# Kernel optimization log

Measured on AMD Instinct MI355X. Metric: run time of the kernel, lower is better.

The kernel has to match this reference:

```python
import jax, jax.numpy as jnp
import numpy as np
import math

D_MODEL = 1024
NUM_HEADS = 16
D_K = D_MODEL // NUM_HEADS
MAX_LEN = 2048
BATCH = 2
SEQ = 2048


def setup_inputs() -> dict:
    key = jax.random.key(0)
    ks = jax.random.split(key, 12)
    w_scale = 0.02  # realistic init scale for linear weights
    inp = {
        "q": jax.random.normal(ks[0], (BATCH, SEQ, D_MODEL), jnp.float32),
        "k": jax.random.normal(ks[1], (BATCH, SEQ, D_MODEL), jnp.float32),
        "v": jax.random.normal(ks[2], (BATCH, SEQ, D_MODEL), jnp.float32),
        # learned params
        "rel_emb": jax.random.normal(ks[3], (2 * MAX_LEN, D_K), jnp.float32),
        "wq": jax.random.normal(ks[4], (D_MODEL, D_MODEL), jnp.float32) * w_scale,
        "bq": jnp.zeros((D_MODEL,), jnp.float32),
        "wk": jax.random.normal(ks[5], (D_MODEL, D_MODEL), jnp.float32) * w_scale,
        "bk": jnp.zeros((D_MODEL,), jnp.float32),
        "wv": jax.random.normal(ks[6], (D_MODEL, D_MODEL), jnp.float32) * w_scale,
        "bv": jnp.zeros((D_MODEL,), jnp.float32),
        "wo": jax.random.normal(ks[7], (D_MODEL, D_MODEL), jnp.float32) * w_scale,
        "bo": jnp.zeros((D_MODEL,), jnp.float32),
    }
    return inp


def reference(q, k, v, rel_emb, wq, bq, wk, bk, wv, bv, wo, bo):
    B, L, D = q.shape
    H, dk = NUM_HEADS, D // NUM_HEADS

    def split_heads(x):  # [B, L, D] -> [B, H, L, dk]
        return x.reshape(B, L, H, dk).transpose(0, 2, 1, 3)

    qh = split_heads(q @ wq.T + bq)
    kh = split_heads(k @ wk.T + bk)
    vh = split_heads(v @ wv.T + bv)

    # relative positions: rel_pos[i, j] = (j - i) + MAX_LEN, in [0, 2*MAX_LEN)
    r = jnp.arange(L)
    rel_pos = r[None, :] - r[:, None] + MAX_LEN  # [L, L] int32

    content_score = jnp.einsum("bhid,bhjd->bhij", qh, kh)
    # pos_score[b,h,i,j] = q[b,h,i,:] . rel_emb[rel_pos[i,j], :]
    rel = rel_emb[rel_pos]  # [L, L, dk]
    pos_score = jnp.einsum("bhid,ijd->bhij", qh, rel)

    scores = (content_score + pos_score) / math.sqrt(dk)
    attn = jax.nn.softmax(scores, axis=-1)
    out = jnp.einsum("bhij,bhjd->bhid", attn, vh)  # [B, H, L, dk]
    out = out.transpose(0, 2, 1, 3).reshape(B, L, D)
    return out @ wo.T + bo
```

## Files before the change

### kernel.cpp

```cpp
#include <hip/hip_runtime.h>
#include <hip/hip_fp16.h>


typedef _Float16 f16;
typedef _Float16 f16x4 __attribute__((ext_vector_type(4)));
typedef _Float16 f16x8 __attribute__((ext_vector_type(8)));
typedef float    f32x4 __attribute__((ext_vector_type(4)));

#define NBATCH 2
#define NHEADS 16
#define DKDIM  64
#define SEQL   2048
#define DMODEL 1024
#define NTOK   4096
#define MAXLEN 2048

__global__ void cvt_f32_f16(const float* __restrict__ src, f16* __restrict__ dst, int n4) {
    int i = blockIdx.x * blockDim.x + threadIdx.x;
    if (i < n4) {
        float4 v = ((const float4*)src)[i];
        f16x4 h = { (f16)v.x, (f16)v.y, (f16)v.z, (f16)v.w };
        ((f16x4*)dst)[i] = h;
    }
}

__global__ __launch_bounds__(256) void qkv_proj(
    const float* __restrict__ qg, const float* __restrict__ kg, const float* __restrict__ vg,
    const float* __restrict__ wq, const float* __restrict__ wk, const float* __restrict__ wv,
    const float* __restrict__ bq, const float* __restrict__ bk, const float* __restrict__ bv,
    f16* __restrict__ qh, f16* __restrict__ kh, f16* __restrict__ vt)
{
    const int which = blockIdx.z;
    const float* X    = which == 0 ? qg : (which == 1 ? kg : vg);
    const float* W    = which == 0 ? wq : (which == 1 ? wk : wv);
    const float* bias = which == 0 ? bq : (which == 1 ? bk : bv);

    __shared__ f16 As[128][72];
    __shared__ f16 Bs[128][72];

    const int tid = threadIdx.x;
    const int lane = tid & 63;
    const int w = tid >> 6;
    const int wr = w >> 1, wc = w & 1;
    const int row0 = blockIdx.y * 128;
    const int col0 = blockIdx.x * 128;

    f32x4 acc[4][4] = {};

    for (int kk = 0; kk < DMODEL; kk += 64) {
        #pragma unroll
        for (int rep = 0; rep < 8; ++rep) {
            int idx = rep * 256 + tid;
            int r = idx >> 4, seg = idx & 15;
            float4 va = *(const float4*)&X[(size_t)(row0 + r) * DMODEL + kk + seg * 4];
            f16x4 ha = { (f16)va.x, (f16)va.y, (f16)va.z, (f16)va.w };
            *(f16x4*)&As[r][seg * 4] = ha;
            float4 vb = *(const float4*)&W[(size_t)(col0 + r) * DMODEL + kk + seg * 4];
            f16x4 hb = { (f16)vb.x, (f16)vb.y, (f16)vb.z, (f16)vb.w };
            *(f16x4*)&Bs[r][seg * 4] = hb;
        }
        __syncthreads();

        f16x8 a[4][2], b[4][2];
        #pragma unroll
        for (int mi = 0; mi < 4; ++mi)
            #pragma unroll
            for (int ks = 0; ks < 2; ++ks)
                a[mi][ks] = *(const f16x8*)&As[wr * 64 + mi * 16 + (lane & 15)][ks * 32 + (lane >> 4) * 8];
        #pragma unroll
        for (int ni = 0; ni < 4; ++ni)
            #pragma unroll
            for (int ks = 0; ks < 2; ++ks)
                b[ni][ks] = *(const f16x8*)&Bs[wc * 64 + ni * 16 + (lane & 15)][ks * 32 + (lane >> 4) * 8];
        __builtin_amdgcn_s_setprio(1);
        #pragma unroll
        for (int mi = 0; mi < 4; ++mi)
            #pragma unroll
            for (int ni = 0; ni < 4; ++ni)
                #pragma unroll
                for (int ks = 0; ks < 2; ++ks)
                    acc[mi][ni] = __builtin_amdgcn_mfma_f32_16x16x32_f16(a[mi][ks], b[ni][ks], acc[mi][ni], 0, 0, 0);
        __builtin_amdgcn_s_setprio(0);
        __syncthreads();
    }

    #pragma unroll
    for (int mi = 0; mi < 4; ++mi) {
        #pragma unroll
        for (int ni = 0; ni < 4; ++ni) {
            int col = col0 + wc * 64 + ni * 16 + (lane & 15);
            int h = col >> 6, d = col & 63;
            float bc = bias[col];
            #pragma unroll
            for (int r = 0; r < 4; ++r) {
                int row = row0 + wr * 64 + mi * 16 + (lane >> 4) * 4 + r;
                int b_ = row >> 11, l = row & 2047;
                float val = acc[mi][ni][r] + bc;
                if (which == 0)
                    qh[((size_t)((b_ * 16 + h) * 2048 + l)) * 64 + d] = (f16)val;
                else if (which == 1)
                    kh[((size_t)((b_ * 16 + h) * 2048 + l)) * 64 + d] = (f16)val;
                else
                    vt[((size_t)((b_ * 16 + h) * 64 + d)) * 2048 + l] = (f16)val;
            }
        }
    }
}

__global__ __launch_bounds__(256, 3) void flash_attn(
    const f16* __restrict__ qh, const f16* __restrict__ kh, const f16* __restrict__ vt,
    const f16* __restrict__ rel, f16* __restrict__ att)
{
    const int tid = threadIdx.x, lane = tid & 63, w = tid >> 6;
    const int bh = blockIdx.y;
    const int b = bh >> 4, h = bh & 15;
    const int i0 = blockIdx.x * 64;

    __shared__ f16 Ks[64][72];
    __shared__ f16 Vs[64][72];
    __shared__ f16 Rb[128][72];
    __shared__ f16 Qb[4][16][88];

    const size_t base_kq = (size_t)bh * SEQL * DKDIM;
    const int pb0 = MAXLEN - i0 - 63;

    #pragma unroll
    for (int rep = 0; rep < 2; ++rep) {
        int idx = rep * 256 + tid;
        int r = idx >> 3, seg = idx & 7;
        *(int4*)&Ks[r][seg * 8] = *(const int4*)&qh[base_kq + (size_t)(i0 + r) * 64 + seg * 8];
        int p = pb0 + r;
        *(int4*)&Rb[p & 127][seg * 8] = *(const int4*)&rel[(size_t)p * 64 + seg * 8];
    }
    __syncthreads();
    f16x8 aq[2];
    aq[0] = *(const f16x8*)&Ks[w * 16 + (lane & 15)][(lane >> 4) * 8];
    aq[1] = *(const f16x8*)&Ks[w * 16 + (lane & 15)][32 + (lane >> 4) * 8];
    __syncthreads();

    float mrun[4], lrun[4];
    f32x4 oacc[4] = {};
    #pragma unroll
    for (int r = 0; r < 4; ++r) { mrun[r] = -1e30f; lrun[r] = 0.f; }

    const int p0w_off = 48 - w * 16;

    for (int j0 = 0; j0 < SEQL; j0 += 64) {
        #pragma unroll
        for (int rep = 0; rep < 2; ++rep) {
            int idx = rep * 256 + tid;
            int r = idx >> 3, seg = idx & 7;
            *(int4*)&Ks[r][seg * 8] = *(const int4*)&kh[base_kq + (size_t)(j0 + r) * 64 + seg * 8];
            *(int4*)&Vs[r][seg * 8] = *(const int4*)&vt[base_kq + (size_t)r * 2048 + j0 + seg * 8];
            int p = pb0 + j0 + 64 + r;
            int slot = p & 127;
            if (p > 4095) p = 4095;
            *(int4*)&Rb[slot][seg * 8] = *(const int4*)&rel[(size_t)p * 64 + seg * 8];
        }
        __syncthreads();

        const int p0w = pb0 + j0 + p0w_off;
        f32x4 sacc[4] = {};
        f32x4 qracc[5] = {};
        __builtin_amdgcn_s_setprio(1);
        #pragma unroll
        for (int nf = 0; nf < 4; ++nf)
            #pragma unroll
            for (int ks = 0; ks < 2; ++ks) {
                f16x8 bk = *(const f16x8*)&Ks[nf * 16 + (lane & 15)][ks * 32 + (lane >> 4) * 8];
                sacc[nf] = __builtin_amdgcn_mfma_f32_16x16x32_f16(aq[ks], bk, sacc[nf], 0, 0, 0);
            }
        #pragma unroll
        for (int pf = 0; pf < 5; ++pf)
            #pragma unroll
            for (int ks = 0; ks < 2; ++ks) {
                f16x8 br = *(const f16x8*)&Rb[(p0w + pf * 16 + (lane & 15)) & 127][ks * 32 + (lane >> 4) * 8];
                qracc[pf] = __builtin_amdgcn_mfma_f32_16x16x32_f16(aq[ks], br, qracc[pf], 0, 0, 0);
            }
        __builtin_amdgcn_s_setprio(0);

        #pragma unroll
        for (int pf = 0; pf < 5; ++pf)
            #pragma unroll
            for (int r = 0; r < 4; ++r)
                Qb[w][(lane >> 4) * 4 + r][pf * 16 + (lane & 15)] = (f16)qracc[pf][r];

        float p_[4][4];
        #pragma unroll
        for (int nf = 0; nf < 4; ++nf)
            #pragma unroll
            for (int r = 0; r < 4; ++r) {
                int gi = (lane >> 4) * 4 + r;
                int c = nf * 16 + (lane & 15) - gi + 15;
                p_[nf][r] = (sacc[nf][r] + (float)Qb[w][gi][c]) * 0.125f;
            }
        float scale[4];
        #pragma unroll
        for (int r = 0; r < 4; ++r) {
            float mx = fmaxf(fmaxf(p_[0][r], p_[1][r]), fmaxf(p_[2][r], p_[3][r]));
            #pragma unroll
            for (int m = 8; m >= 1; m >>= 1) mx = fmaxf(mx, __shfl_xor(mx, m, 64));
            float mnew = fmaxf(mrun[r], mx);
            scale[r] = __expf(mrun[r] - mnew);
            float sm = 0.f;
            #pragma unroll
            for (int nf = 0; nf < 4; ++nf) { p_[nf][r] = __expf(p_[nf][r] - mnew); sm += p_[nf][r]; }
            #pragma unroll
            for (int m = 8; m >= 1; m >>= 1) sm += __shfl_xor(sm, m, 64);
            lrun[r] = lrun[r] * scale[r] + sm;
            mrun[r] = mnew;
        }
        #pragma unroll
        for (int df = 0; df < 4; ++df)
            #pragma unroll
            for (int r = 0; r < 4; ++r) oacc[df][r] *= scale[r];

        #pragma unroll
        for (int nf = 0; nf < 4; ++nf)
            #pragma unroll
            for (int r = 0; r < 4; ++r)
                Qb[w][(lane >> 4) * 4 + r][nf * 16 + (lane & 15)] = (f16)p_[nf][r];
        f16x8 pa[2];
        pa[0] = *(const f16x8*)&Qb[w][lane & 15][(lane >> 4) * 8];
        pa[1] = *(const f16x8*)&Qb[w][lane & 15][32 + (lane >> 4) * 8];
        __builtin_amdgcn_s_setprio(1);
        #pragma unroll
        for (int df = 0; df < 4; ++df)
            #pragma unroll
            for (int ks = 0; ks < 2; ++ks) {
                f16x8 bv = *(const f16x8*)&Vs[df * 16 + (lane & 15)][ks * 32 + (lane >> 4) * 8];
                oacc[df] = __builtin_amdgcn_mfma_f32_16x16x32_f16(pa[ks], bv, oacc[df], 0, 0, 0);
            }
        __builtin_amdgcn_s_setprio(0);
        __syncthreads();
    }

    #pragma unroll
    for (int df = 0; df < 4; ++df) {
        int d = df * 16 + (lane & 15);
        #pragma unroll
        for (int r = 0; r < 4; ++r) {
            int i = i0 + w * 16 + (lane >> 4) * 4 + r;
            float val = oacc[df][r] / lrun[r];
            att[((size_t)(b * 2048 + i)) * DMODEL + h * 64 + d] = (f16)val;
        }
    }
}

__global__ __launch_bounds__(256) void out_proj(
    const f16* __restrict__ att, const f16* __restrict__ wo16, const float* __restrict__ bo,
    float* __restrict__ out)
{
    __shared__ f16 As[128][72];
    __shared__ f16 Bs[128][72];
    const int tid = threadIdx.x, lane = tid & 63, w = tid >> 6;
    const int wr = w >> 1, wc = w & 1;
    const int row0 = blockIdx.y * 128, col0 = blockIdx.x * 128;

    f32x4 acc[4][4] = {};

    for (int kk = 0; kk < DMODEL; kk += 64) {
        #pragma unroll
        for (int rep = 0; rep < 4; ++rep) {
            int idx = rep * 256 + tid;
            int r = idx >> 3, seg = idx & 7;
            *(int4*)&As[r][seg * 8] = *(const int4*)&att[(size_t)(row0 + r) * DMODEL + kk + seg * 8];
            *(int4*)&Bs[r][seg * 8] = *(const int4*)&wo16[(size_t)(col0 + r) * DMODEL + kk + seg * 8];
        }
        __syncthreads();

        f16x8 a[4][2], b[4][2];
        #pragma unroll
        for (int mi = 0; mi < 4; ++mi)
            #pragma unroll
            for (int ks = 0; ks < 2; ++ks)
                a[mi][ks] = *(const f16x8*)&As[wr * 64 + mi * 16 + (lane & 15)][ks * 32 + (lane >> 4) * 8];
        #pragma unroll
        for (int ni = 0; ni < 4; ++ni)
            #pragma unroll
            for (int ks = 0; ks < 2; ++ks)
                b[ni][ks] = *(const f16x8*)&Bs[wc * 64 + ni * 16 + (lane & 15)][ks * 32 + (lane >> 4) * 8];
        __builtin_amdgcn_s_setprio(1);
        #pragma unroll
        for (int mi = 0; mi < 4; ++mi)
            #pragma unroll
            for (int ni = 0; ni < 4; ++ni)
                #pragma unroll
                for (int ks = 0; ks < 2; ++ks)
                    acc[mi][ni] = __builtin_amdgcn_mfma_f32_16x16x32_f16(a[mi][ks], b[ni][ks], acc[mi][ni], 0, 0, 0);
        __builtin_amdgcn_s_setprio(0);
        __syncthreads();
    }

    #pragma unroll
    for (int mi = 0; mi < 4; ++mi)
        #pragma unroll
        for (int ni = 0; ni < 4; ++ni) {
            int col = col0 + wc * 64 + ni * 16 + (lane & 15);
            float bc = bo[col];
            #pragma unroll
            for (int r = 0; r < 4; ++r) {
                int row = row0 + wr * 64 + mi * 16 + (lane >> 4) * 4 + r;
                out[(size_t)row * DMODEL + col] = acc[mi][ni][r] + bc;
            }
        }
}

extern "C" void kernel_launch(void* const* d_in, const int* in_sizes, int n_in,
                              void* d_out, int out_size, void* d_ws, size_t ws_size,
                              hipStream_t stream) {
    const float* q   = (const float*)d_in[0];
    const float* k   = (const float*)d_in[1];
    const float* v   = (const float*)d_in[2];
    const float* rel = (const float*)d_in[3];
    const float* wq  = (const float*)d_in[4];
    const float* bq  = (const float*)d_in[5];
    const float* wk  = (const float*)d_in[6];
    const float* bk  = (const float*)d_in[7];
    const float* wv  = (const float*)d_in[8];
    const float* bv  = (const float*)d_in[9];
    const float* wo  = (const float*)d_in[10];
    const float* bo  = (const float*)d_in[11];
    float* out = (float*)d_out;

    f16* ws    = (f16*)d_ws;
    f16* wo16  = ws;
    f16* rel16 = wo16 + (size_t)DMODEL * DMODEL;
    f16* qh16  = rel16 + (size_t)2 * MAXLEN * DKDIM;
    f16* kh16  = qh16 + (size_t)NTOK * DMODEL;
    f16* vt16  = kh16 + (size_t)NTOK * DMODEL;
    f16* att16 = vt16 + (size_t)NTOK * DMODEL;

    cvt_f32_f16<<<dim3(1024), 256, 0, stream>>>(wo, wo16, DMODEL * DMODEL / 4);
    cvt_f32_f16<<<dim3(256),  256, 0, stream>>>(rel, rel16, 2 * MAXLEN * DKDIM / 4);
    qkv_proj<<<dim3(8, 32, 3), 256, 0, stream>>>(q, k, v, wq, wk, wv, bq, bk, bv,
                                                 qh16, kh16, vt16);
    flash_attn<<<dim3(32, 32), 256, 0, stream>>>(qh16, kh16, vt16, rel16, att16);
    out_proj<<<dim3(8, 32), 256, 0, stream>>>(att16, wo16, bo, out);
}
```

Measured before the change: 394.4 us.

## Register-prefetch global tiles, transpose attention MFMAs, fuse wo conversion into out_proj

Adds register double-buffering to qkv_proj, flash_attn and out_proj, so the next tile's global loads are issued before the current tile's MFMAs and latency is hidden. Flash attention swaps the MFMA operand order so each lane owns one query row; softmax reductions then need fewer shuffles and the score and P stores to LDS become packed vector writes. The V projection epilogue writes the transposed output as packed f16x4, and out_proj converts fp32 wo on the fly, which removes a separate conversion kernel. The extra prefetch registers raise register pressure and may lower occupancy despite the launch-bound hints.

Result: slower. 470.5 us (+19.3%).

```diff
diff --git a/kernel.cpp b/kernel.cpp
--- a/kernel.cpp
+++ b/kernel.cpp
@@ -24,7 +24,7 @@
     }
 }
 
-__global__ __launch_bounds__(256) void qkv_proj(
+__global__ __launch_bounds__(256, 2) void qkv_proj(
     const float* __restrict__ qg, const float* __restrict__ kg, const float* __restrict__ vg,
     const float* __restrict__ wq, const float* __restrict__ wk, const float* __restrict__ wv,
     const float* __restrict__ bq, const float* __restrict__ bk, const float* __restrict__ bv,
@@ -46,21 +46,36 @@
     const int col0 = blockIdx.x * 128;
 
     f32x4 acc[4][4] = {};
+    float4 ra[8], rw[8];
+
+    #pragma unroll
+    for (int rep = 0; rep < 8; ++rep) {
+        int idx = rep * 256 + tid;
+        int r = idx >> 4, seg = idx & 15;
+        ra[rep] = *(const float4*)&X[(size_t)(row0 + r) * DMODEL + seg * 4];
+        rw[rep] = *(const float4*)&W[(size_t)(col0 + r) * DMODEL + seg * 4];
+    }
 
     for (int kk = 0; kk < DMODEL; kk += 64) {
         #pragma unroll
         for (int rep = 0; rep < 8; ++rep) {
             int idx = rep * 256 + tid;
             int r = idx >> 4, seg = idx & 15;
-            float4 va = *(const float4*)&X[(size_t)(row0 + r) * DMODEL + kk + seg * 4];
-            f16x4 ha = { (f16)va.x, (f16)va.y, (f16)va.z, (f16)va.w };
+            f16x4 ha = { (f16)ra[rep].x, (f16)ra[rep].y, (f16)ra[rep].z, (f16)ra[rep].w };
             *(f16x4*)&As[r][seg * 4] = ha;
-            float4 vb = *(const float4*)&W[(size_t)(col0 + r) * DMODEL + kk + seg * 4];
-            f16x4 hb = { (f16)vb.x, (f16)vb.y, (f16)vb.z, (f16)vb.w };
+            f16x4 hb = { (f16)rw[rep].x, (f16)rw[rep].y, (f16)rw[rep].z, (f16)rw[rep].w };
             *(f16x4*)&Bs[r][seg * 4] = hb;
         }
         __syncthreads();
-
+        if (kk + 64 < DMODEL) {
+            #pragma unroll
+            for (int rep = 0; rep < 8; ++rep) {
+                int idx = rep * 256 + tid;
+                int r = idx >> 4, seg = idx & 15;
+                ra[rep] = *(const float4*)&X[(size_t)(row0 + r) * DMODEL + kk + 64 + seg * 4];
+                rw[rep] = *(const float4*)&W[(size_t)(col0 + r) * DMODEL + kk + 64 + seg * 4];
+            }
+        }
         f16x8 a[4][2], b[4][2];
         #pragma unroll
         for (int mi = 0; mi < 4; ++mi)
@@ -91,17 +106,17 @@
             int col = col0 + wc * 64 + ni * 16 + (lane & 15);
             int h = col >> 6, d = col & 63;
             float bc = bias[col];
-            #pragma unroll
-            for (int r = 0; r < 4; ++r) {
-                int row = row0 + wr * 64 + mi * 16 + (lane >> 4) * 4 + r;
-                int b_ = row >> 11, l = row & 2047;
-                float val = acc[mi][ni][r] + bc;
-                if (which == 0)
-                    qh[((size_t)((b_ * 16 + h) * 2048 + l)) * 64 + d] = (f16)val;
-                else if (which == 1)
-                    kh[((size_t)((b_ * 16 + h) * 2048 + l)) * 64 + d] = (f16)val;
-                else
-                    vt[((size_t)((b_ * 16 + h) * 64 + d)) * 2048 + l] = (f16)val;
+            int rowb = row0 + wr * 64 + mi * 16 + (lane >> 4) * 4;
+            int b_ = rowb >> 11, l0 = rowb & 2047;
+            if (which == 2) {
+                f16x4 pk = { (f16)(acc[mi][ni][0] + bc), (f16)(acc[mi][ni][1] + bc),
+                             (f16)(acc[mi][ni][2] + bc), (f16)(acc[mi][ni][3] + bc) };
+                *(f16x4*)&vt[((size_t)((b_ * 16 + h) * 64 + d)) * 2048 + l0] = pk;
+            } else {
+                f16* dst = (which == 0) ? qh : kh;
+                #pragma unroll
+                for (int r = 0; r < 4; ++r)
+                    dst[((size_t)((b_ * 16 + h) * 2048 + l0 + r)) * 64 + d] = (f16)(acc[mi][ni][r] + bc);
             }
         }
     }
@@ -112,6 +127,7 @@
     const f16* __restrict__ rel, f16* __restrict__ att)
 {
     const int tid = threadIdx.x, lane = tid & 63, w = tid >> 6;
+    const int i_l = lane & 15, hi = lane >> 4;
     const int bh = blockIdx.y;
     const int b = bh >> 4, h = bh & 15;
     const int i0 = blockIdx.x * 64;
@@ -134,15 +150,23 @@
     }
     __syncthreads();
     f16x8 aq[2];
-    aq[0] = *(const f16x8*)&Ks[w * 16 + (lane & 15)][(lane >> 4) * 8];
-    aq[1] = *(const f16x8*)&Ks[w * 16 + (lane & 15)][32 + (lane >> 4) * 8];
+    aq[0] = *(const f16x8*)&Ks[w * 16 + i_l][hi * 8];
+    aq[1] = *(const f16x8*)&Ks[w * 16 + i_l][32 + hi * 8];
+
+    int4 rk[2], rv[2], rr[2];
+    #pragma unroll
+    for (int rep = 0; rep < 2; ++rep) {
+        int idx = rep * 256 + tid;
+        int r = idx >> 3, seg = idx & 7;
+        rk[rep] = *(const int4*)&kh[base_kq + (size_t)r * 64 + seg * 8];
+        rv[rep] = *(const int4*)&vt[base_kq + (size_t)r * 2048 + seg * 8];
+        int p = pb0 + 64 + r; if (p > 4095) p = 4095;
+        rr[rep] = *(const int4*)&rel[(size_t)p * 64 + seg * 8];
+    }
     __syncthreads();
 
-    float mrun[4], lrun[4];
+    float mrun = -1e30f, lrun = 0.f;
     f32x4 oacc[4] = {};
-    #pragma unroll
-    for (int r = 0; r < 4; ++r) { mrun[r] = -1e30f; lrun[r] = 0.f; }
-
     const int p0w_off = 48 - w * 16;
 
     for (int j0 = 0; j0 < SEQL; j0 += 64) {
@@ -150,105 +174,127 @@
         for (int rep = 0; rep < 2; ++rep) {
             int idx = rep * 256 + tid;
             int r = idx >> 3, seg = idx & 7;
-            *(int4*)&Ks[r][seg * 8] = *(const int4*)&kh[base_kq + (size_t)(j0 + r) * 64 + seg * 8];
-            *(int4*)&Vs[r][seg * 8] = *(const int4*)&vt[base_kq + (size_t)r * 2048 + j0 + seg * 8];
-            int p = pb0 + j0 + 64 + r;
-            int slot = p & 127;
-            if (p > 4095) p = 4095;
-            *(int4*)&Rb[slot][seg * 8] = *(const int4*)&rel[(size_t)p * 64 + seg * 8];
-        }
-        __syncthreads();
+            *(int4*)&Ks[r][seg * 8] = rk[rep];
+            *(int4*)&Vs[r][seg * 8] = rv[rep];
+            *(int4*)&Rb[(pb0 + j0 + 64 + r) & 127][seg * 8] = rr[rep];
+        }
+        __syncthreads();
+
+        if (j0 + 64 < SEQL) {
+            #pragma unroll
+            for (int rep = 0; rep < 2; ++rep) {
+                int idx = rep * 256 + tid;
+                int r = idx >> 3, seg = idx & 7;
+                rk[rep] = *(const int4*)&kh[base_kq + (size_t)(j0 + 64 + r) * 64 + seg * 8];
+                rv[rep] = *(const int4*)&vt[base_kq + (size_t)r * 2048 + j0 + 64 + seg * 8];
+                int p = pb0 + j0 + 128 + r;
+                int slot_p = p; if (slot_p > 4095) slot_p = 4095;
+                rr[rep] = *(const int4*)&rel[(size_t)slot_p * 64 + seg * 8];
+            }
+        }
 
         const int p0w = pb0 + j0 + p0w_off;
         f32x4 sacc[4] = {};
         f32x4 qracc[5] = {};
         __builtin_amdgcn_s_setprio(1);
         #pragma unroll
+        for (int jf = 0; jf < 4; ++jf)
+            #pragma unroll
+            for (int ks = 0; ks < 2; ++ks) {
+                f16x8 ak = *(const f16x8*)&Ks[jf * 16 + i_l][ks * 32 + hi * 8];
+                sacc[jf] = __builtin_amdgcn_mfma_f32_16x16x32_f16(ak, aq[ks], sacc[jf], 0, 0, 0);
+            }
+        #pragma unroll
+        for (int pf = 0; pf < 5; ++pf)
+            #pragma unroll
+            for (int ks = 0; ks < 2; ++ks) {
+                f16x8 ar = *(const f16x8*)&Rb[(p0w + pf * 16 + i_l) & 127][ks * 32 + hi * 8];
+                qracc[pf] = __builtin_amdgcn_mfma_f32_16x16x32_f16(ar, aq[ks], qracc[pf], 0, 0, 0);
+            }
+        __builtin_amdgcn_s_setprio(0);
+
+        #pragma unroll
+        for (int pf = 0; pf < 5; ++pf) {
+            f16x4 pk = { (f16)qracc[pf][0], (f16)qracc[pf][1], (f16)qracc[pf][2], (f16)qracc[pf][3] };
+            *(f16x4*)&Qb[w][i_l][pf * 16 + 4 * hi] = pk;
+        }
+
+        float p_[4][4];
+        #pragma unroll
         for (int nf = 0; nf < 4; ++nf)
             #pragma unroll
+            for (int r = 0; r < 4; ++r) {
+                int t = nf * 16 + 4 * hi + r - i_l + 15;
+                p_[nf][r] = (sacc[nf][r] + (float)Qb[w][i_l][t]) * 0.125f;
+            }
+
+        float mx = fmaxf(fmaxf(fmaxf(p_[0][0], p_[0][1]), fmaxf(p_[0][2], p_[0][3])),
+                         fmaxf(fmaxf(p_[1][0], p_[1][1]), fmaxf(p_[1][2], p_[1][3])));
+        mx = fmaxf(mx, fmaxf(fmaxf(fmaxf(p_[2][0], p_[2][1]), fmaxf(p_[2][2], p_[2][3])),
+                             fmaxf(fmaxf(p_[3][0], p_[3][1]), fmaxf(p_[3][2], p_[3][3]))));
+        mx = fmaxf(mx, __shfl_xor(mx, 16, 64));
+        mx = fmaxf(mx, __shfl_xor(mx, 32, 64));
+        float mnew = fmaxf(mrun, mx);
+        float sc = __expf(mrun - mnew);
+        float sm = 0.f;
+        #pragma unroll
+        for (int nf = 0; nf < 4; ++nf) {
+            #pragma unroll
+            for (int r = 0; r < 4; ++r) { p_[nf][r] = __expf(p_[nf][r] - mnew); }
+            sm += (p_[nf][0] + p_[nf][1]) + (p_[nf][2] + p_[nf][3]);
+        }
+        sm += __shfl_xor(sm, 16, 64);
+        sm += __shfl_xor(sm, 32, 64);
+        lrun = lrun * sc + sm;
+        mrun = mnew;
+
+        float scb[4];
+        #pragma unroll
+        for (int r = 0; r < 4; ++r)
+            scb[r] = __shfl(sc, (lane & 48) | (4 * hi + r), 64);
+        #pragma unroll
+        for (int df = 0; df < 4; ++df)
+            #pragma unroll
+            for (int r = 0; r < 4; ++r) oacc[df][r] *= scb[r];
+
+        #pragma unroll
+        for (int nf = 0; nf < 4; ++nf) {
+            f16x4 pk = { (f16)p_[nf][0], (f16)p_[nf][1], (f16)p_[nf][2], (f16)p_[nf][3] };
+            *(f16x4*)&Qb[w][i_l][nf * 16 + 4 * hi] = pk;
+        }
+        f16x8 pa[2];
+        pa[0] = *(const f16x8*)&Qb[w][i_l][hi * 8];
+        pa[1] = *(const f16x8*)&Qb[w][i_l][32 + hi * 8];
+        __builtin_amdgcn_s_setprio(1);
+        #pragma unroll
+        for (int df = 0; df < 4; ++df)
+            #pragma unroll
             for (int ks = 0; ks < 2; ++ks) {
-                f16x8 bk = *(const f16x8*)&Ks[nf * 16 + (lane & 15)][ks * 32 + (lane >> 4) * 8];
-                sacc[nf] = __builtin_amdgcn_mfma_f32_16x16x32_f16(aq[ks], bk, sacc[nf], 0, 0, 0);
-            }
-        #pragma unroll
-        for (int pf = 0; pf < 5; ++pf)
-            #pragma unroll
-            for (int ks = 0; ks < 2; ++ks) {
-                f16x8 br = *(const f16x8*)&Rb[(p0w + pf * 16 + (lane & 15)) & 127][ks * 32 + (lane >> 4) * 8];
-                qracc[pf] = __builtin_amdgcn_mfma_f32_16x16x32_f16(aq[ks], br, qracc[pf], 0, 0, 0);
+                f16x8 bv = *(const f16x8*)&Vs[df * 16 + i_l][ks * 32 + hi * 8];
+                oacc[df] = __builtin_amdgcn_mfma_f32_16x16x32_f16(pa[ks], bv, oacc[df], 0, 0, 0);
             }
         __builtin_amdgcn_s_setprio(0);
-
-        #pragma unroll
-        for (int pf = 0; pf < 5; ++pf)
-            #pragma unroll
-            for (int r = 0; r < 4; ++r)
-                Qb[w][(lane >> 4) * 4 + r][pf * 16 + (lane & 15)] = (f16)qracc[pf][r];
-
-        float p_[4][4];
-        #pragma unroll
-        for (int nf = 0; nf < 4; ++nf)
-            #pragma unroll
-            for (int r = 0; r < 4; ++r) {
-                int gi = (lane >> 4) * 4 + r;
-                int c = nf * 16 + (lane & 15) - gi + 15;
-                p_[nf][r] = (sacc[nf][r] + (float)Qb[w][gi][c]) * 0.125f;
-            }
-        float scale[4];
+        __syncthreads();
+    }
+
+    float lb[4];
+    #pragma unroll
+    for (int r = 0; r < 4; ++r)
+        lb[r] = __shfl(lrun, (lane & 48) | (4 * hi + r), 64);
+    #pragma unroll
+    for (int df = 0; df < 4; ++df) {
+        int d = df * 16 + i_l;
         #pragma unroll
         for (int r = 0; r < 4; ++r) {
-            float mx = fmaxf(fmaxf(p_[0][r], p_[1][r]), fmaxf(p_[2][r], p_[3][r]));
-            #pragma unroll
-            for (int m = 8; m >= 1; m >>= 1) mx = fmaxf(mx, __shfl_xor(mx, m, 64));
-            float mnew = fmaxf(mrun[r], mx);
-            scale[r] = __expf(mrun[r] - mnew);
-            float sm = 0.f;
-            #pragma unroll
-            for (int nf = 0; nf < 4; ++nf) { p_[nf][r] = __expf(p_[nf][r] - mnew); sm += p_[nf][r]; }
-            #pragma unroll
-            for (int m = 8; m >= 1; m >>= 1) sm += __shfl_xor(sm, m, 64);
-            lrun[r] = lrun[r] * scale[r] + sm;
-            mrun[r] = mnew;
-        }
-        #pragma unroll
-        for (int df = 0; df < 4; ++df)
-            #pragma unroll
-            for (int r = 0; r < 4; ++r) oacc[df][r] *= scale[r];
-
-        #pragma unroll
-        for (int nf = 0; nf < 4; ++nf)
-            #pragma unroll
-            for (int r = 0; r < 4; ++r)
-                Qb[w][(lane >> 4) * 4 + r][nf * 16 + (lane & 15)] = (f16)p_[nf][r];
-        f16x8 pa[2];
-        pa[0] = *(const f16x8*)&Qb[w][lane & 15][(lane >> 4) * 8];
-        pa[1] = *(const f16x8*)&Qb[w][lane & 15][32 + (lane >> 4) * 8];
-        __builtin_amdgcn_s_setprio(1);
-        #pragma unroll
-        for (int df = 0; df < 4; ++df)
-            #pragma unroll
-            for (int ks = 0; ks < 2; ++ks) {
-                f16x8 bv = *(const f16x8*)&Vs[df * 16 + (lane & 15)][ks * 32 + (lane >> 4) * 8];
-                oacc[df] = __builtin_amdgcn_mfma_f32_16x16x32_f16(pa[ks], bv, oacc[df], 0, 0, 0);
-            }
-        __builtin_amdgcn_s_setprio(0);
-        __syncthreads();
-    }
-
-    #pragma unroll
-    for (int df = 0; df < 4; ++df) {
-        int d = df * 16 + (lane & 15);
-        #pragma unroll
-        for (int r = 0; r < 4; ++r) {
-            int i = i0 + w * 16 + (lane >> 4) * 4 + r;
-            float val = oacc[df][r] / lrun[r];
+            int i = i0 + w * 16 + 4 * hi + r;
+            float val = oacc[df][r] / lb[r];
             att[((size_t)(b * 2048 + i)) * DMODEL + h * 64 + d] = (f16)val;
         }
     }
 }
 
-__global__ __launch_bounds__(256) void out_proj(
-    const f16* __restrict__ att, const f16* __restrict__ wo16, const float* __restrict__ bo,
+__global__ __launch_bounds__(256, 2) void out_proj(
+    const f16* __restrict__ att, const float* __restrict__ wo, const float* __restrict__ bo,
     float* __restrict__ out)
 {
     __shared__ f16 As[128][72];
@@ -258,17 +304,51 @@
     const int row0 = blockIdx.y * 128, col0 = blockIdx.x * 128;
 
     f32x4 acc[4][4] = {};
+    int4 pa_[4];
+    float4 pw[8];
+
+    #pragma unroll
+    for (int rep = 0; rep < 4; ++rep) {
+        int idx = rep * 256 + tid;
+        int r = idx >> 3, seg = idx & 7;
+        pa_[rep] = *(const int4*)&att[(size_t)(row0 + r) * DMODEL + seg * 8];
+    }
+    #pragma unroll
+    for (int rep = 0; rep < 8; ++rep) {
+        int idx = rep * 256 + tid;
+        int r = idx >> 4, seg = idx & 15;
+        pw[rep] = *(const float4*)&wo[(size_t)(col0 + r) * DMODEL + seg * 4];
+    }
 
     for (int kk = 0; kk < DMODEL; kk += 64) {
         #pragma unroll
         for (int rep = 0; rep < 4; ++rep) {
             int idx = rep * 256 + tid;
             int r = idx >> 3, seg = idx & 7;
-            *(int4*)&As[r][seg * 8] = *(const int4*)&att[(size_t)(row0 + r) * DMODEL + kk + seg * 8];
-            *(int4*)&Bs[r][seg * 8] = *(const int4*)&wo16[(size_t)(col0 + r) * DMODEL + kk + seg * 8];
-        }
-        __syncthreads();
-
+            *(int4*)&As[r][seg * 8] = pa_[rep];
+        }
+        #pragma unroll
+        for (int rep = 0; rep < 8; ++rep) {
+            int idx = rep * 256 + tid;
+            int r = idx >> 4, seg = idx & 15;
+            f16x4 hb = { (f16)pw[rep].x, (f16)pw[rep].y, (f16)pw[rep].z, (f16)pw[rep].w };
+            *(f16x4*)&Bs[r][seg * 4] = hb;
+        }
+        __syncthreads();
+        if (kk + 64 < DMODEL) {
+            #pragma unroll
+            for (int rep = 0; rep < 4; ++rep) {
+                int idx = rep * 256 + tid;
+                int r = idx >> 3, seg = idx & 7;
+                pa_[rep] = *(const int4*)&att[(size_t)(row0 + r) * DMODEL + kk + 64 + seg * 8];
+            }
+            #pragma unroll
+            for (int rep = 0; rep < 8; ++rep) {
+                int idx = rep * 256 + tid;
+                int r = idx >> 4, seg = idx & 15;
+                pw[rep] = *(const float4*)&wo[(size_t)(col0 + r) * DMODEL + kk + 64 + seg * 4];
+            }
+        }
         f16x8 a[4][2], b[4][2];
         #pragma unroll
         for (int mi = 0; mi < 4; ++mi)
@@ -324,17 +404,15 @@
     float* out = (float*)d_out;
 
     f16* ws    = (f16*)d_ws;
-    f16* wo16  = ws;
-    f16* rel16 = wo16 + (size_t)DMODEL * DMODEL;
+    f16* rel16 = ws;
     f16* qh16  = rel16 + (size_t)2 * MAXLEN * DKDIM;
     f16* kh16  = qh16 + (size_t)NTOK * DMODEL;
     f16* vt16  = kh16 + (size_t)NTOK * DMODEL;
     f16* att16 = vt16 + (size_t)NTOK * DMODEL;
 
-    cvt_f32_f16<<<dim3(1024), 256, 0, stream>>>(wo, wo16, DMODEL * DMODEL / 4);
-    cvt_f32_f16<<<dim3(256),  256, 0, stream>>>(rel, rel16, 2 * MAXLEN * DKDIM / 4);
+    cvt_f32_f16<<<dim3(256), 256, 0, stream>>>(rel, rel16, 2 * MAXLEN * DKDIM / 4);
     qkv_proj<<<dim3(8, 32, 3), 256, 0, stream>>>(q, k, v, wq, wk, wv, bq, bk, bv,
                                                  qh16, kh16, vt16);
     flash_attn<<<dim3(32, 32), 256, 0, stream>>>(qh16, kh16, vt16, rel16, att16);
-    out_proj<<<dim3(8, 32), 256, 0, stream>>>(att16, wo16, bo, out);
+    out_proj<<<dim3(8, 32), 256, 0, stream>>>(att16, wo, bo, out);
 }
```
